# Kernel optimization log

Hardware: AMD Instinct MI355X
Metric: run time of the kernel (lower is better)

Reference implementation:

```python
import jax, jax.numpy as jnp
import numpy as np

N_QUBITS = 9
N_LAYERS = 4
EPS = 1e-5


def _apply_ry(state, wire, theta):
    # state: [N, 2**n] real; theta: [N] or scalar
    n = N_QUBITS
    N = state.shape[0]
    left, right = 2 ** wire, 2 ** (n - 1 - wire)
    s = state.reshape(N, left, 2, right)
    th = jnp.broadcast_to(jnp.asarray(theta, state.dtype), (N,))[:, None, None]
    c, si = jnp.cos(th / 2), jnp.sin(th / 2)
    a, b = s[:, :, 0, :], s[:, :, 1, :]
    out = jnp.stack([c * a - si * b, si * a + c * b], axis=2)
    return out.reshape(N, -1)


def _apply_cnot(state, ctrl, tgt):
    n = N_QUBITS
    N = state.shape[0]
    s = state.reshape((N,) + (2,) * n)
    ca, ta = ctrl + 1, tgt + 1
    sub = jnp.take(s, 1, axis=ca)          # control == 1 slice
    ta2 = ta - 1 if ta > ca else ta
    sub = jnp.flip(sub, axis=ta2)          # X on target
    idx = [slice(None)] * (n + 1)
    idx[ca] = 1
    s = s.at[tuple(idx)].set(sub)
    return s.reshape(N, -1)


def quantum_layer(inputs, q_weights):
    # inputs: [N, n_qubits] angles; q_weights: [n_layers, n_qubits]
    N = inputs.shape[0]
    state = jnp.zeros((N, 2 ** N_QUBITS), inputs.dtype).at[:, 0].set(1.0)
    for i in range(N_QUBITS):
        state = _apply_ry(state, i, inputs[:, i])
    for j in range(N_LAYERS):
        for i in range(N_QUBITS):
            state = _apply_cnot(state, i, (i + 1) % N_QUBITS)
        for i in range(N_QUBITS):
            state = _apply_ry(state, i, q_weights[j, i])
    probs = (state * state).reshape((N,) + (2,) * N_QUBITS)
    zs = []
    for i in range(N_QUBITS):
        axes = tuple(a for a in range(1, N_QUBITS + 1) if a != i + 1)
        p = probs.sum(axes)                # [N, 2]
        zs.append(p[:, 0] - p[:, 1])
    return jnp.stack(zs, axis=1)           # [N, n_qubits]


def _bn(x):
    mu = x.mean((0, 2, 3), keepdims=True)
    var = x.var((0, 2, 3), keepdims=True)
    return (x - mu) * jax.lax.rsqrt(var + EPS)


def _maxpool(x, kh, kw):
    return jax.lax.reduce_window(x, -jnp.inf, jax.lax.max,
                                 (1, 1, kh, kw), (1, 1, kh, kw), 'VALID')


def _conv(x, w):
    return jax.lax.conv_general_dilated(x, w, (1, 1), 'VALID',
                                        dimension_numbers=('NCHW', 'OIHW', 'NCHW'))


def _forward(x, w_conv1, w_conv2, w_conv3, q_weights, fc_w, fc_b):
    h = jax.nn.elu(_bn(_conv(x, w_conv1)))
    h = jnp.pad(h, ((0, 0), (0, 0), (0, 1), (16, 17)))     # ZeroPad2d(16,17,0,1)
    h = _maxpool(jax.nn.elu(_bn(_conv(h, w_conv2))), 2, 4)
    h = jnp.pad(h, ((0, 0), (0, 0), (4, 3), (2, 1)))       # ZeroPad2d(2,1,4,3)
    h = _maxpool(jax.nn.elu(_bn(_conv(h, w_conv3))), 2, 4)
    B, C = h.shape[0], h.shape[1]
    feats = h.reshape(B, C, -1)                            # [B, 32, 9]
    q = quantum_layer(feats.reshape(B * C, N_QUBITS), q_weights)
    q = q.reshape(B, C * N_QUBITS)                         # channel-major concat
    return q @ fc_w.T + fc_b


def setup_inputs() -> dict:
    key = jax.random.key(0)
    ks = jax.random.split(key, 7)
    return {
        'x': jax.random.normal(ks[0], (1024, 1, 4, 216), jnp.float32),
        'w_conv1': jax.random.normal(ks[1], (16, 1, 1, 64), jnp.float32) * 0.05,
        'w_conv2': jax.random.normal(ks[2], (32, 16, 2, 32), jnp.float32) * 0.05,
        'w_conv3': jax.random.normal(ks[3], (32, 32, 8, 4), jnp.float32) * 0.05,
        'q_weights': jax.random.uniform(ks[4], (N_LAYERS, N_QUBITS), jnp.float32, 0.0, 2 * np.pi),
        'fc_w': jax.random.normal(ks[5], (5, 32 * N_QUBITS), jnp.float32) * 0.05,
        'fc_b': jnp.zeros((5,), jnp.float32),
    }


def reference(x, w_conv1, w_conv2, w_conv3, q_weights, fc_w, fc_b):
    return _forward(x, w_conv1, w_conv2, w_conv3, q_weights, fc_w, fc_b)
```

## Files before the change

### kernel.cpp

```cpp
#include <hip/hip_runtime.h>
#include <math.h>

#define NB 1024
#define C1 16
#define H1 4
#define W1 153
#define WX 216
#define K1 64
#define C2 32
#define H2 4
#define W2 155
#define W192 192
#define PW2 38
#define C3 32
#define W3 38

typedef short short4v __attribute__((ext_vector_type(4)));
typedef short short8 __attribute__((ext_vector_type(8)));
typedef float f32x16 __attribute__((ext_vector_type(16)));

#define OFF_OUT1     0
#define OFF_A1H      10027008
#define OFF_A1L      16318464
#define OFF_W2PH     22609920
#define OFF_W2PL     22626304
#define OFF_W3PH     22642688
#define OFF_W3PL     22659072
#define OFF_UH       22675456
#define OFF_UL       22806528
#define OFF_POOL2RAW 22937600
#define OFF_A2H      25427968
#define OFF_A2L      27787264
#define OFF_FEATSRAW 30146560
#define OFF_QO       30441472
#define OFF_PART1    30736384
#define OFF_PART2    30867456
#define OFF_PART3    30998528
#define OFF_STATS1   31031296
#define OFF_STATS2   31031328
#define OFF_STATS3   31031392

__device__ __forceinline__ float eluf(float x){ return x > 0.f ? x : expm1f(x); }

__device__ __forceinline__ ushort bf16h(float x){
  unsigned u = __float_as_uint(x);
  unsigned r = u + 0x7fffu + ((u >> 16) & 1u);
  return (ushort)(r >> 16);
}
__device__ __forceinline__ float bf16f(ushort h){ return __uint_as_float(((unsigned)h) << 16); }

__device__ __forceinline__ short8 cat8(short4v a, short4v b){
  return __builtin_shufflevector(a, b, 0,1,2,3,4,5,6,7);
}

__global__ __launch_bounds__(256) void k_conv1s(const float* __restrict__ x,
                                                const float* __restrict__ w1,
                                                float* __restrict__ out1,
                                                float* __restrict__ part1){
  __shared__ float xr[4][WX];
  __shared__ float wl[C1*K1];
  int n = blockIdx.x, tid = threadIdx.x;
  for (int i = tid; i < 4*WX; i += 256) xr[i/WX][i%WX] = x[(size_t)n*4*WX + i];
  for (int i = tid; i < C1*K1; i += 256) wl[i] = w1[i];
  __syncthreads();
  int h = tid >> 6, lane = tid & 63;
  float acc[16][3];
  #pragma unroll
  for (int c = 0; c < 16; ++c){ acc[c][0]=0.f; acc[c][1]=0.f; acc[c][2]=0.f; }
  bool v2 = (lane + 128) < W1;
  for (int k = 0; k < 64; ++k){
    float x0 = xr[h][lane + k];
    float x1 = xr[h][lane + 64 + k];
    float x2 = v2 ? xr[h][lane + 128 + k] : 0.f;
    #pragma unroll
    for (int c = 0; c < 16; ++c){
      float wk = wl[c*64 + k];
      acc[c][0] += wk*x0; acc[c][1] += wk*x1; acc[c][2] += wk*x2;
    }
  }
  float ss[16], sq[16];
  #pragma unroll
  for (int c = 0; c < 16; ++c){
    float* ob = out1 + (((size_t)(n*16 + c)*4 + h))*W1;
    ob[lane] = acc[c][0];
    ob[lane + 64] = acc[c][1];
    if (v2) ob[lane + 128] = acc[c][2];
    ss[c] = acc[c][0] + acc[c][1] + acc[c][2];
    sq[c] = acc[c][0]*acc[c][0] + acc[c][1]*acc[c][1] + acc[c][2]*acc[c][2];
  }
  #pragma unroll
  for (int m = 1; m < 64; m <<= 1){
    #pragma unroll
    for (int c = 0; c < 16; ++c){ ss[c] += __shfl_xor(ss[c], m); sq[c] += __shfl_xor(sq[c], m); }
  }
  if (lane == 0){
    #pragma unroll
    for (int c = 0; c < 16; ++c){
      part1[((size_t)(n*4 + h)*16 + c)*2]     = ss[c];
      part1[((size_t)(n*4 + h)*16 + c)*2 + 1] = sq[c];
    }
  }
}

__global__ __launch_bounds__(256) void k_stats_finP(const float* __restrict__ part,
                                                    float* __restrict__ stats,
                                                    int C, int nblk, float inv){
  __shared__ float rs[256], rq[256];
  int c = blockIdx.x;
  float s = 0.f, q = 0.f;
  for (int b = threadIdx.x; b < nblk; b += 256){
    s += part[((size_t)b*C + c)*2];
    q += part[((size_t)b*C + c)*2 + 1];
  }
  rs[threadIdx.x] = s; rq[threadIdx.x] = q; __syncthreads();
  for (int st = 128; st > 0; st >>= 1){
    if (threadIdx.x < st){ rs[threadIdx.x] += rs[threadIdx.x+st]; rq[threadIdx.x] += rq[threadIdx.x+st]; }
    __syncthreads();
  }
  if (threadIdx.x == 0){
    float mean = rs[0]*inv;
    float var  = rq[0]*inv - mean*mean;
    stats[c*2]   = mean;
    stats[c*2+1] = rsqrtf(var + 1e-5f);
  }
}

__global__ __launch_bounds__(256) void k_bnelu1(const float* __restrict__ out1,
                                                const float* __restrict__ stats,
                                                ushort* __restrict__ a1h, ushort* __restrict__ a1l){
  __shared__ float xf[2448];
  __shared__ float st[32];
  int b = blockIdx.x;
  int n = b >> 2, h = b & 3;
  int tid = threadIdx.x;
  if (tid < 32) st[tid] = stats[tid];
  for (int i = tid; i < 2448; i += 256){
    int ci = i / 153, w = i - ci*153;
    xf[i] = out1[((size_t)(n*16 + ci)*4 + h)*W1 + w];
  }
  __syncthreads();
  for (int i = tid; i < 3072; i += 256){
    int w = i >> 4, ci = i & 15;
    float v = 0.f;
    int ws = w - 16;
    if ((unsigned)ws < (unsigned)W1){
      float xx = xf[ci*153 + ws];
      v = eluf((xx - st[ci*2])*st[ci*2+1]);
    }
    int ciS = ci ^ (((w >> 2) & 3) << 2);
    size_t o = (size_t)b*3072 + w*16 + ciS;
    ushort hs = bf16h(v);
    a1h[o] = hs;
    a1l[o] = bf16h(v - bf16f(hs));
  }
}

__global__ void k_cvtw(const float* __restrict__ w2, const float* __restrict__ w3,
                       ushort* __restrict__ w2ph, ushort* __restrict__ w2pl,
                       ushort* __restrict__ w3ph, ushort* __restrict__ w3pl){
  int idx = blockIdx.x*256 + threadIdx.x;
  if (idx < 32768){
    int ci = idx & 15; int co = (idx >> 4) & 31; int rk = idx >> 9;
    int r = rk >> 5, kw = rk & 31;
    float v = w2[((size_t)(co*16 + ci)*2 + r)*32 + kw];
    ushort hs = bf16h(v); float hf = bf16f(hs);
    w2ph[idx] = hs; w2pl[idx] = bf16h(v - hf);
  } else {
    int j = idx - 32768;
    int ci = j & 31; int co = (j >> 5) & 31; int rk = j >> 10;
    int r = rk >> 2, kw = rk & 3;
    float v = w3[((size_t)(co*32 + ci)*8 + r)*4 + kw];
    ushort hs = bf16h(v); float hf = bf16f(hs);
    w3ph[j] = hs; w3pl[j] = bf16h(v - hf);
  }
}

template<int HG, int PS>
__device__ __forceinline__ void conv2_body(const ushort* s_hi, const ushort* s_lo,
                                           const ushort* __restrict__ w2ph,
                                           const ushort* __restrict__ w2pl,
                                           float* __restrict__ pool2raw,
                                           float (*statW)[32][2],
                                           int n, int l31, int l5){
  constexpr int P0 = PS ? 3 : 0;
  constexpr int NP = PS ? 2 : 3;
  constexpr int NR = (HG == 0) ? 3 : 2;

  f32x16 acc[2][NP];
  #pragma unroll
  for (int lh = 0; lh < 2; ++lh)
    #pragma unroll
    for (int p = 0; p < NP; ++p)
      #pragma unroll
      for (int e = 0; e < 16; ++e) acc[lh][p][e] = 0.f;

  for (int kw = 0; kw < 32; ++kw){
    short8 Ah[2], Al[2];
    #pragma unroll
    for (int r = 0; r < 2; ++r){
      int widx = ((r*32 + kw)*32 + l31)*16 + l5*4;
      Ah[r] = cat8(*(const short4v*)(w2ph + widx), *(const short4v*)(w2ph + widx + 8));
      Al[r] = cat8(*(const short4v*)(w2pl + widx), *(const short4v*)(w2pl + widx + 8));
    }
    #pragma unroll
    for (int j = 0; j < NR; ++j){
      int rb = (2*HG + j)*3072;
      short8 bh[NP], bl[NP];
      #pragma unroll
      for (int p = 0; p < NP; ++p){
        int pos = (P0 + p)*32 + l31 + kw;
        int sw = ((pos >> 2) & 3) << 2;
        int off0 = rb + pos*16 + ((l5*4) ^ sw);
        int off1 = rb + pos*16 + ((l5*4 + 8) ^ sw);
        bh[p] = cat8(*(const short4v*)(s_hi + off0), *(const short4v*)(s_hi + off1));
        bl[p] = cat8(*(const short4v*)(s_lo + off0), *(const short4v*)(s_lo + off1));
      }
      #pragma unroll
      for (int lh = 0; lh < 2; ++lh){
        #pragma unroll
        for (int r = 0; r < 2; ++r){
          if (lh + r != j) continue;
          #pragma unroll
          for (int p = 0; p < NP; ++p){
            acc[lh][p] = __builtin_amdgcn_mfma_f32_32x32x16_bf16(Ah[r], bh[p], acc[lh][p], 0, 0, 0);
            acc[lh][p] = __builtin_amdgcn_mfma_f32_32x32x16_bf16(Ah[r], bl[p], acc[lh][p], 0, 0, 0);
            acc[lh][p] = __builtin_amdgcn_mfma_f32_32x32x16_bf16(Al[r], bh[p], acc[lh][p], 0, 0, 0);
          }
        }
      }
    }
  }

  {
    float sreg[16], qreg[16];
    #pragma unroll
    for (int e = 0; e < 16; ++e){ sreg[e] = 0.f; qreg[e] = 0.f; }
    #pragma unroll
    for (int lh = 0; lh < 2; ++lh){
      #pragma unroll
      for (int p = 0; p < NP; ++p){
        bool pv = ((P0 + p) < 4) || (l31 < 27);
        #pragma unroll
        for (int e = 0; e < 16; ++e){
          float v = pv ? acc[lh][p][e] : 0.f;
          sreg[e] += v; qreg[e] += v*v;
        }
      }
    }
    #pragma unroll
    for (int m = 1; m < 32; m <<= 1){
      #pragma unroll
      for (int e = 0; e < 16; ++e){
        sreg[e] += __shfl_xor(sreg[e], m);
        qreg[e] += __shfl_xor(qreg[e], m);
      }
    }
    if (l31 == 0){
      #pragma unroll
      for (int e = 0; e < 16; ++e){
        int co = (e & 3) + ((e >> 2) << 3) + (l5 << 2);
        statW[HG*2 + PS][co][0] = sreg[e];
        statW[HG*2 + PS][co][1] = qreg[e];
      }
    }
  }
  #pragma unroll
  for (int p = 0; p < NP; ++p){
    #pragma unroll
    for (int e = 0; e < 16; ++e){
      float m0 = fmaxf(acc[0][p][e], acc[1][p][e]);
      float v1 = fmaxf(m0, __shfl_xor(m0, 1));
      float v2m = fmaxf(v1, __shfl_xor(v1, 2));
      int pw = (P0 + p)*8 + (l31 >> 2);
      if ((l31 & 3) == 0 && pw < PW2){
        int co = (e & 3) + ((e >> 2) << 3) + (l5 << 2);
        pool2raw[(((size_t)n*2 + HG)*32 + co)*PW2 + pw] = v2m;
      }
    }
  }
}

__global__ __launch_bounds__(256) void k_conv2f(const ushort* __restrict__ a1h,
                                                const ushort* __restrict__ a1l,
                                                const ushort* __restrict__ w2ph,
                                                const ushort* __restrict__ w2pl,
                                                float* __restrict__ pool2raw,
                                                float* __restrict__ part2){
  __shared__ __align__(16) ushort s_hi[4*3072];
  __shared__ __align__(16) ushort s_lo[4*3072];
  __shared__ float statW[4][32][2];
  int n = blockIdx.x;
  int tid = threadIdx.x;
  {
    const float4* gh = (const float4*)(a1h + (size_t)n*12288);
    const float4* gl = (const float4*)(a1l + (size_t)n*12288);
    float4* dh = (float4*)s_hi;
    float4* dl = (float4*)s_lo;
    #pragma unroll
    for (int i = 0; i < 6; ++i){ dh[tid + 256*i] = gh[tid + 256*i]; dl[tid + 256*i] = gl[tid + 256*i]; }
  }
  __syncthreads();
  int wv = tid >> 6, lane = tid & 63;
  int l5 = lane >> 5, l31 = lane & 31;
  int role = (wv + n) & 3;
  switch (role){
    case 0: conv2_body<0,0>(s_hi, s_lo, w2ph, w2pl, pool2raw, statW, n, l31, l5); break;
    case 1: conv2_body<0,1>(s_hi, s_lo, w2ph, w2pl, pool2raw, statW, n, l31, l5); break;
    case 2: conv2_body<1,0>(s_hi, s_lo, w2ph, w2pl, pool2raw, statW, n, l31, l5); break;
    default: conv2_body<1,1>(s_hi, s_lo, w2ph, w2pl, pool2raw, statW, n, l31, l5); break;
  }
  __syncthreads();
  if (tid < 64){
    int hg = tid >> 5, co = tid & 31;
    float s = statW[hg*2][co][0] + statW[hg*2 + 1][co][0];
    float q = statW[hg*2][co][1] + statW[hg*2 + 1][co][1];
    part2[(((size_t)n*2 + hg)*32 + co)*2]     = s;
    part2[(((size_t)n*2 + hg)*32 + co)*2 + 1] = q;
  }
}

__global__ __launch_bounds__(256) void k_bn2(const float* __restrict__ pool2raw,
                                             const float* __restrict__ stats,
                                             ushort* __restrict__ a2h, ushort* __restrict__ a2l){
  __shared__ float xf[1216];
  __shared__ float st[64];
  int b = blockIdx.x;
  int tid = threadIdx.x;
  if (tid < 64) st[tid] = stats[tid];
  for (int i = tid; i < 1216; i += 256) xf[i] = pool2raw[(size_t)b*1216 + i];
  __syncthreads();
  for (int i = tid; i < 2304; i += 256){
    int w = i >> 5, ci = i & 31;
    float v = 0.f;
    int pw = w - 2;
    if ((unsigned)pw < (unsigned)PW2)
      v = eluf((xf[ci*38 + pw] - st[ci*2])*st[ci*2+1]);
    int ciS = ci ^ (((w >> 1) & 7) << 2);
    size_t o = (size_t)b*2304 + w*32 + ciS;
    ushort hs = bf16h(v);
    a2h[o] = hs; a2l[o] = bf16h(v - bf16f(hs));
  }
}

__global__ __launch_bounds__(256, 2) void k_conv3f(const ushort* __restrict__ a2h,
                                                   const ushort* __restrict__ a2l,
                                                   const ushort* __restrict__ w3ph,
                                                   const ushort* __restrict__ w3pl,
                                                   float* __restrict__ featsraw,
                                                   float* __restrict__ part3){
  __shared__ __align__(16) ushort s3h[9216];
  __shared__ __align__(16) ushort s3l[9216];
  __shared__ float poolL3[4][32][12];
  __shared__ float statL3[4][32][2];
  int nb = blockIdx.x;
  int tid = threadIdx.x;
  {
    const float4* gh = (const float4*)(a2h + (size_t)nb*9216);
    const float4* gl = (const float4*)(a2l + (size_t)nb*9216);
    float4* dh = (float4*)s3h;
    float4* dl = (float4*)s3l;
    for (int i = tid; i < 1152; i += 256){ dh[i] = gh[i]; dl[i] = gl[i]; }
  }
  __syncthreads();
  int wave = tid >> 6, lane = tid & 63;
  int nh = wave >> 1, h = wave & 1;
  int l5 = lane >> 5, l31 = lane & 31;

  f32x16 acc[2];
  #pragma unroll
  for (int p = 0; p < 2; ++p)
    #pragma unroll
    for (int e = 0; e < 16; ++e) acc[p][e] = 0.f;

  #pragma unroll
  for (int ri = 0; ri < 2; ++ri){
    int r = (h == 0) ? (4 + ri) : (3 + ri);
    int rbase = (nh*2 + ri)*72*32;
    #pragma unroll
    for (int kw = 0; kw < 4; ++kw){
      #pragma unroll
      for (int ch = 0; ch < 2; ++ch){
        int widx = ((r*4 + kw)*32 + l31)*32 + ch*16 + l5*4;
        short8 Ah = cat8(*(const short4v*)(w3ph + widx), *(const short4v*)(w3ph + widx + 8));
        short8 Al = cat8(*(const short4v*)(w3pl + widx), *(const short4v*)(w3pl + widx + 8));
        short8 Bh[2], Bl[2];
        #pragma unroll
        for (int p = 0; p < 2; ++p){
          int pos = p*32 + l31 + kw;
          int sw = ((pos >> 1) & 7) << 2;
          int s0 = ch*16 + l5*4;
          int off0 = rbase + pos*32 + (s0 ^ sw);
          int off1 = rbase + pos*32 + ((s0 + 8) ^ sw);
          Bh[p] = cat8(*(const short4v*)(s3h + off0), *(const short4v*)(s3h + off1));
          Bl[p] = cat8(*(const short4v*)(s3l + off0), *(const short4v*)(s3l + off1));
        }
        #pragma unroll
        for (int p = 0; p < 2; ++p) acc[p] = __builtin_amdgcn_mfma_f32_32x32x16_bf16(Ah, Bh[p], acc[p], 0, 0, 0);
        #pragma unroll
        for (int p = 0; p < 2; ++p) acc[p] = __builtin_amdgcn_mfma_f32_32x32x16_bf16(Ah, Bl[p], acc[p], 0, 0, 0);
        #pragma unroll
        for (int p = 0; p < 2; ++p) acc[p] = __builtin_amdgcn_mfma_f32_32x32x16_bf16(Al, Bh[p], acc[p], 0, 0, 0);
      }
    }
  }

  {
    float sreg[16], qreg[16];
    #pragma unroll
    for (int e = 0; e < 16; ++e){ sreg[e] = 0.f; qreg[e] = 0.f; }
    #pragma unroll
    for (int p = 0; p < 2; ++p){
      bool pv = (p == 0) || (l31 < 6);
      #pragma unroll
      for (int e = 0; e < 16; ++e){
        float v = pv ? acc[p][e] : 0.f;
        sreg[e] += v; qreg[e] += v*v;
      }
    }
    #pragma unroll
    for (int m = 1; m < 32; m <<= 1){
      #pragma unroll
      for (int e = 0; e < 16; ++e){
        sreg[e] += __shfl_xor(sreg[e], m);
        qreg[e] += __shfl_xor(qreg[e], m);
      }
    }
    if (l31 == 0){
      #pragma unroll
      for (int e = 0; e < 16; ++e){
        int co = (e & 3) + ((e >> 2) << 3) + (l5 << 2);
        statL3[wave][co][0] = sreg[e];
        statL3[wave][co][1] = qreg[e];
      }
    }
  }
  #pragma unroll
  for (int p = 0; p < 2; ++p){
    #pragma unroll
    for (int e = 0; e < 16; ++e){
      float v = acc[p][e];
      float v1 = fmaxf(v, __shfl_xor(v, 1));
      float v2m = fmaxf(v1, __shfl_xor(v1, 2));
      int pw = p*8 + (l31 >> 2);
      if ((l31 & 3) == 0 && pw < 9){
        int co = (e & 3) + ((e >> 2) << 3) + (l5 << 2);
        poolL3[wave][co][pw] = v2m;
      }
    }
  }
  __syncthreads();
  for (int i = tid; i < 2*32*9; i += 256){
    int pw = i % 9; int t = i / 9; int co = t & 31; int nh2 = t >> 5;
    float v = fmaxf(poolL3[nh2*2][co][pw], poolL3[nh2*2+1][co][pw]);
    featsraw[((size_t)(nb*2 + nh2)*32 + co)*9 + pw] = v;
  }
  if (tid < 32){
    float s = 0.f, q = 0.f;
    #pragma unroll
    for (int wv = 0; wv < 4; ++wv){ s += statL3[wv][tid][0]; q += statL3[wv][tid][1]; }
    part3[((size_t)nb*32 + tid)*2]     = s;
    part3[((size_t)nb*32 + tid)*2 + 1] = q;
  }
}

__global__ __launch_bounds__(256) void k_buildU(const float* __restrict__ qw,
                                                ushort* __restrict__ Uh, ushort* __restrict__ Ul){
  __shared__ float wt[36][2];
  int tid = threadIdx.x;
  if (tid < 36){ float s, c; sincosf(qw[tid]*0.5f, &s, &c); wt[tid][0] = c; wt[tid][1] = s; }
  __syncthreads();
  int wid = tid >> 6, lane = tid & 63;
  int k = blockIdx.x*4 + wid;
  float v[8];
  #pragma unroll
  for (int r = 0; r < 8; ++r) v[r] = (lane*8 + r == k) ? 1.f : 0.f;

  for (int j = 0; j < 4; ++j){
    #pragma unroll
    for (int i = 0; i < 5; ++i){
      int cm = 32>>i, tm = 16>>i;
      bool flip = (lane & cm) != 0;
      #pragma unroll
      for (int r = 0; r < 8; ++r){
        float w = __shfl_xor(v[r], tm);
        v[r] = flip ? w : v[r];
      }
    }
    { bool flip = (lane & 1) != 0;
      #pragma unroll
      for (int r = 0; r < 4; ++r){ float a = v[r], bb = v[r+4]; v[r] = flip?bb:a; v[r+4] = flip?a:bb; } }
    { float t = v[4]; v[4] = v[6]; v[6] = t; t = v[5]; v[5] = v[7]; v[7] = t; }
    { float t = v[2]; v[2] = v[3]; v[3] = t; t = v[6]; v[6] = v[7]; v[7] = t; }
    #pragma unroll
    for (int r = 1; r < 8; r += 2) v[r] = __shfl_xor(v[r], 32);

    #pragma unroll
    for (int i = 0; i < 6; ++i){
      float c = wt[j*9+i][0], s = wt[j*9+i][1];
      int m = 32>>i;
      float sg = (lane & m) ? s : -s;
      #pragma unroll
      for (int r = 0; r < 8; ++r){
        float w = __shfl_xor(v[r], m);
        v[r] = c*v[r] + sg*w;
      }
    }
    { float c = wt[j*9+6][0], s = wt[j*9+6][1];
      #pragma unroll
      for (int r = 0; r < 4; ++r){ float a = v[r], bb = v[r+4]; v[r] = c*a - s*bb; v[r+4] = s*a + c*bb; } }
    { float c = wt[j*9+7][0], s = wt[j*9+7][1]; float a, bb;
      a=v[0]; bb=v[2]; v[0]=c*a-s*bb; v[2]=s*a+c*bb;
      a=v[1]; bb=v[3]; v[1]=c*a-s*bb; v[3]=s*a+c*bb;
      a=v[4]; bb=v[6]; v[4]=c*a-s*bb; v[6]=s*a+c*bb;
      a=v[5]; bb=v[7]; v[5]=c*a-s*bb; v[7]=s*a+c*bb; }
    { float c = wt[j*9+8][0], s = wt[j*9+8][1]; float a, bb;
      a=v[0]; bb=v[1]; v[0]=c*a-s*bb; v[1]=s*a+c*bb;
      a=v[2]; bb=v[3]; v[2]=c*a-s*bb; v[3]=s*a+c*bb;
      a=v[4]; bb=v[5]; v[4]=c*a-s*bb; v[5]=s*a+c*bb;
      a=v[6]; bb=v[7]; v[6]=c*a-s*bb; v[7]=s*a+c*bb; }
  }
  #pragma unroll
  for (int r = 0; r < 8; ++r){
    int s = lane*8 + r;
    int mf = s >> 5, r31 = s & 31;
    int addr = (((k >> 4)*16 + mf)*32 + r31)*16 + (k & 15);
    float f = v[r];
    ushort hi = bf16h(f);
    Uh[addr] = hi;
    Ul[addr] = bf16h(f - bf16f(hi));
  }
}

__global__ __launch_bounds__(256, 1) void k_qgemm(const float* __restrict__ featsraw,
                                                  const float* __restrict__ stats,
                                                  const ushort* __restrict__ Uh,
                                                  const ushort* __restrict__ Ul,
                                                  float* __restrict__ qo){
  __shared__ __align__(16) ushort BhL[32768];
  __shared__ __align__(16) ushort BlL[32768];
  __shared__ float angL[576];
  __shared__ float zred[4][64][9];
  int nb = blockIdx.x;
  int tid = threadIdx.x;
  for (int t = tid; t < 576; t += 256){
    float vr = featsraw[(size_t)nb*576 + t];
    int c = (t/9) & 31;
    angL[t] = 0.5f * eluf((vr - stats[c*2])*stats[c*2+1]);
  }
  __syncthreads();
  {
    int sm = tid >> 2, q = tid & 3;
    float tc[9], ts[9];
    #pragma unroll
    for (int i = 0; i < 9; ++i) sincosf(angL[sm*9 + i], &ts[i], &tc[i]);
    float Pc = ((q & 2) ? ts[0] : tc[0]) * ((q & 1) ? ts[1] : tc[1]);
    int swz = (sm >> 2) & 3;
    short4v* bh4 = (short4v*)BhL;
    short4v* bl4 = (short4v*)BlL;
    int j = 0;
    #pragma unroll
    for (int b2 = 0; b2 < 2; ++b2){ float p2 = Pc*(b2 ? ts[2] : tc[2]);
    #pragma unroll
    for (int b3 = 0; b3 < 2; ++b3){ float p3 = p2*(b3 ? ts[3] : tc[3]);
    #pragma unroll
    for (int b4 = 0; b4 < 2; ++b4){ float p4 = p3*(b4 ? ts[4] : tc[4]);
    #pragma unroll
    for (int b5 = 0; b5 < 2; ++b5){ float p5 = p4*(b5 ? ts[5] : tc[5]);
    #pragma unroll
    for (int b6 = 0; b6 < 2; ++b6){ float p6 = p5*(b6 ? ts[6] : tc[6]);
      float a0 = p6*tc[7]*tc[8];
      float a1 = p6*tc[7]*ts[8];
      float a2 = p6*ts[7]*tc[8];
      float a3 = p6*ts[7]*ts[8];
      ushort h0 = bf16h(a0), h1 = bf16h(a1), h2 = bf16h(a2), h3 = bf16h(a3);
      short4v hv; hv[0]=(short)h0; hv[1]=(short)h1; hv[2]=(short)h2; hv[3]=(short)h3;
      short4v lv; lv[0]=(short)bf16h(a0 - bf16f(h0)); lv[1]=(short)bf16h(a1 - bf16f(h1));
                  lv[2]=(short)bf16h(a2 - bf16f(h2)); lv[3]=(short)bf16h(a3 - bf16f(h3));
      int kk = q*128 + j;
      int kstep = kk >> 4;
      int g = (kk >> 2) & 3;
      int idx4 = (kstep*64 + sm)*4 + (g ^ swz);
      bh4[idx4] = hv; bl4[idx4] = lv;
      j += 4;
    }}}}}
  }
  __syncthreads();
  int wv = tid >> 6, lane = tid & 63, l5 = lane >> 5, l31 = lane & 31;
  f32x16 acc[4][2];
  #pragma unroll
  for (int jj = 0; jj < 4; ++jj)
    #pragma unroll
    for (int nf = 0; nf < 2; ++nf)
      #pragma unroll
      for (int e = 0; e < 16; ++e) acc[jj][nf][e] = 0.f;

  for (int kstep = 0; kstep < 32; ++kstep){
    short8 Bh[2], Bl[2];
    #pragma unroll
    for (int nf = 0; nf < 2; ++nf){
      int sm = nf*32 + l31;
      int base = (kstep*64 + sm)*16;
      int sz = ((sm >> 2) & 3) << 2;
      int e0 = (l5*4) ^ sz;
      int e1 = (l5*4 + 8) ^ sz;
      Bh[nf] = cat8(*(const short4v*)(BhL + base + e0), *(const short4v*)(BhL + base + e1));
      Bl[nf] = cat8(*(const short4v*)(BlL + base + e0), *(const short4v*)(BlL + base + e1));
    }
    #pragma unroll
    for (int jj = 0; jj < 4; ++jj){
      int mf = wv*4 + jj;
      const ushort* ah = Uh + ((kstep*16 + mf)*32 + l31)*16 + l5*4;
      const ushort* al = Ul + ((kstep*16 + mf)*32 + l31)*16 + l5*4;
      short8 Ah = cat8(*(const short4v*)ah, *(const short4v*)(ah + 8));
      short8 Al = cat8(*(const short4v*)al, *(const short4v*)(al + 8));
      acc[jj][0] = __builtin_amdgcn_mfma_f32_32x32x16_bf16(Ah, Bh[0], acc[jj][0], 0, 0, 0);
      acc[jj][1] = __builtin_amdgcn_mfma_f32_32x32x16_bf16(Ah, Bh[1], acc[jj][1], 0, 0, 0);
      acc[jj][0] = __builtin_amdgcn_mfma_f32_32x32x16_bf16(Ah, Bl[0], acc[jj][0], 0, 0, 0);
      acc[jj][1] = __builtin_amdgcn_mfma_f32_32x32x16_bf16(Ah, Bl[1], acc[jj][1], 0, 0, 0);
      acc[jj][0] = __builtin_amdgcn_mfma_f32_32x32x16_bf16(Al, Bh[0], acc[jj][0], 0, 0, 0);
      acc[jj][1] = __builtin_amdgcn_mfma_f32_32x32x16_bf16(Al, Bh[1], acc[jj][1], 0, 0, 0);
    }
  }
  float zz[2][9];
  #pragma unroll
  for (int nf = 0; nf < 2; ++nf)
    #pragma unroll
    for (int i = 0; i < 9; ++i) zz[nf][i] = 0.f;
  #pragma unroll
  for (int jj = 0; jj < 4; ++jj){
    int mf = wv*4 + jj;
    float sg0 = (mf & 8) ? -1.f : 1.f;
    float sg1 = (mf & 4) ? -1.f : 1.f;
    float sg2 = (mf & 2) ? -1.f : 1.f;
    float sg3 = (mf & 1) ? -1.f : 1.f;
    #pragma unroll
    for (int nf = 0; nf < 2; ++nf){
      float psum = 0.f, z4 = 0.f, z5 = 0.f, z7 = 0.f, z8 = 0.f;
      #pragma unroll
      for (int e = 0; e < 16; ++e){
        float qv = acc[jj][nf][e]*acc[jj][nf][e];
        psum += qv;
        z4 += ((e >> 3) & 1) ? -qv : qv;
        z5 += ((e >> 2) & 1) ? -qv : qv;
        z7 += ((e >> 1) & 1) ? -qv : qv;
        z8 += (e & 1) ? -qv : qv;
      }
      zz[nf][0] += sg0*psum; zz[nf][1] += sg1*psum;
      zz[nf][2] += sg2*psum; zz[nf][3] += sg3*psum;
      zz[nf][4] += z4; zz[nf][5] += z5;
      zz[nf][6] += l5 ? -psum : psum;
      zz[nf][7] += z7; zz[nf][8] += z8;
    }
  }
  #pragma unroll
  for (int nf = 0; nf < 2; ++nf)
    #pragma unroll
    for (int i = 0; i < 9; ++i) zz[nf][i] += __shfl_xor(zz[nf][i], 32);
  if (l5 == 0){
    #pragma unroll
    for (int nf = 0; nf < 2; ++nf)
      #pragma unroll
      for (int i = 0; i < 9; ++i) zred[wv][nf*32 + l31][i] = zz[nf][i];
  }
  __syncthreads();
  for (int t = tid; t < 576; t += 256){
    int sm = t / 9, i = t - sm*9;
    float s = zred[0][sm][i] + zred[1][sm][i] + zred[2][sm][i] + zred[3][sm][i];
    qo[(size_t)(nb*64 + sm)*9 + i] = s;
  }
}

__global__ void k_fc(const float* __restrict__ q, const float* __restrict__ fw,
                     const float* __restrict__ fb, float* __restrict__ out){
  int idx = blockIdx.x*256 + threadIdx.x;
  if (idx >= NB*5) return;
  int b = idx / 5, o = idx - b*5;
  const float* qr = q + (size_t)b*288;
  const float* wr = fw + (size_t)o*288;
  float s = 0.f;
  for (int j = 0; j < 288; ++j) s += qr[j]*wr[j];
  out[idx] = s + fb[o];
}

extern "C" void kernel_launch(void* const* d_in, const int* in_sizes, int n_in,
                              void* d_out, int out_size, void* d_ws, size_t ws_size,
                              hipStream_t stream){
  const float* x  = (const float*)d_in[0];
  const float* w1 = (const float*)d_in[1];
  const float* w2 = (const float*)d_in[2];
  const float* w3 = (const float*)d_in[3];
  const float* qw = (const float*)d_in[4];
  const float* fw = (const float*)d_in[5];
  const float* fb = (const float*)d_in[6];
  float* out = (float*)d_out;
  float* W = (float*)d_ws;

  float*  out1   = W + OFF_OUT1;
  ushort* a1h    = (ushort*)(W + OFF_A1H);
  ushort* a1l    = (ushort*)(W + OFF_A1L);
  ushort* w2ph   = (ushort*)(W + OFF_W2PH);
  ushort* w2pl   = (ushort*)(W + OFF_W2PL);
  ushort* w3ph   = (ushort*)(W + OFF_W3PH);
  ushort* w3pl   = (ushort*)(W + OFF_W3PL);
  ushort* uH     = (ushort*)(W + OFF_UH);
  ushort* uL     = (ushort*)(W + OFF_UL);
  float*  pool2raw = W + OFF_POOL2RAW;
  ushort* a2h    = (ushort*)(W + OFF_A2H);
  ushort* a2l    = (ushort*)(W + OFF_A2L);
  float*  featsraw = W + OFF_FEATSRAW;
  float*  qo     = W + OFF_QO;
  float*  part1  = W + OFF_PART1;
  float*  part2  = W + OFF_PART2;
  float*  part3  = W + OFF_PART3;
  float*  stats1 = W + OFF_STATS1;
  float*  stats2 = W + OFF_STATS2;
  float*  stats3 = W + OFF_STATS3;

  k_conv1s<<<NB, 256, 0, stream>>>(x, w1, out1, part1);
  k_stats_finP<<<16, 256, 0, stream>>>(part1, stats1, 16, NB*4, 1.f/((float)NB*H1*W1));
  k_bnelu1<<<NB*4, 256, 0, stream>>>(out1, stats1, a1h, a1l);
  k_cvtw<<<256, 256, 0, stream>>>(w2, w3, w2ph, w2pl, w3ph, w3pl);
  k_buildU<<<128, 256, 0, stream>>>(qw, uH, uL);
  k_conv2f<<<NB, 256, 0, stream>>>(a1h, a1l, w2ph, w2pl, pool2raw, part2);
  k_stats_finP<<<32, 256, 0, stream>>>(part2, stats2, 32, NB*2, 1.f/((float)NB*H2*W2));
  k_bn2<<<NB*2, 256, 0, stream>>>(pool2raw, stats2, a2h, a2l);
  k_conv3f<<<NB/2, 256, 0, stream>>>(a2h, a2l, w3ph, w3pl, featsraw, part3);
  k_stats_finP<<<32, 256, 0, stream>>>(part3, stats3, 32, NB/2, 1.f/((float)NB*2*W3));
  k_qgemm<<<NB/2, 256, 0, stream>>>(featsraw, stats3, uH, uL, qo);
  k_fc<<<20, 256, 0, stream>>>(qo, fw, fb, out);
}
```

Before: 338.2 us.

## Split conv2 blocks per height group and widen LDS loads to 16 bytes

The conv2 kernel now launches two blocks per sample, one per output height group. Each block loads only the 3 or 2 input rows it needs into LDS, so shared memory per block shrinks and occupancy can rise. The position tiles are spread across four waves per block with finer granularity. The LDS swizzle is changed to an 8-element XOR so the A and B operands load as single 16-byte short8 reads instead of two 8-byte reads. The risk is redundant staging of the overlapping middle row and uneven work among the four waves.

```diff
diff --git a/kernel.cpp b/kernel.cpp
--- a/kernel.cpp
+++ b/kernel.cpp
@@ -147,7 +147,7 @@
       float xx = xf[ci*153 + ws];
       v = eluf((xx - st[ci*2])*st[ci*2+1]);
     }
-    int ciS = ci ^ (((w >> 2) & 3) << 2);
+    int ciS = ci ^ (((w >> 2) & 1) << 3);
     size_t o = (size_t)b*3072 + w*16 + ciS;
     ushort hs = bf16h(v);
     a1h[o] = hs;
@@ -182,9 +182,10 @@
                                            float* __restrict__ pool2raw,
                                            float (*statW)[32][2],
                                            int n, int l31, int l5){
-  constexpr int P0 = PS ? 3 : 0;
-  constexpr int NP = PS ? 2 : 3;
+  constexpr int P0 = (PS == 0) ? 0 : (PS + 1);
+  constexpr int NP = (PS == 0) ? 2 : 1;
   constexpr int NR = (HG == 0) ? 3 : 2;
+  int e8 = l5*8;
 
   f32x16 acc[2][NP];
   #pragma unroll
@@ -198,22 +199,20 @@
     short8 Ah[2], Al[2];
     #pragma unroll
     for (int r = 0; r < 2; ++r){
-      int widx = ((r*32 + kw)*32 + l31)*16 + l5*4;
-      Ah[r] = cat8(*(const short4v*)(w2ph + widx), *(const short4v*)(w2ph + widx + 8));
-      Al[r] = cat8(*(const short4v*)(w2pl + widx), *(const short4v*)(w2pl + widx + 8));
+      int widx = ((r*32 + kw)*32 + l31)*16 + e8;
+      Ah[r] = *(const short8*)(w2ph + widx);
+      Al[r] = *(const short8*)(w2pl + widx);
     }
     #pragma unroll
     for (int j = 0; j < NR; ++j){
-      int rb = (2*HG + j)*3072;
+      int rb = j*3072;
       short8 bh[NP], bl[NP];
       #pragma unroll
       for (int p = 0; p < NP; ++p){
         int pos = (P0 + p)*32 + l31 + kw;
-        int sw = ((pos >> 2) & 3) << 2;
-        int off0 = rb + pos*16 + ((l5*4) ^ sw);
-        int off1 = rb + pos*16 + ((l5*4 + 8) ^ sw);
-        bh[p] = cat8(*(const short4v*)(s_hi + off0), *(const short4v*)(s_hi + off1));
-        bl[p] = cat8(*(const short4v*)(s_lo + off0), *(const short4v*)(s_lo + off1));
+        int off = rb + pos*16 + (e8 ^ (((pos >> 2) & 1) << 3));
+        bh[p] = *(const short8*)(s_hi + off);
+        bl[p] = *(const short8*)(s_lo + off);
       }
       #pragma unroll
       for (int lh = 0; lh < 2; ++lh){
@@ -259,8 +258,8 @@
       #pragma unroll
       for (int e = 0; e < 16; ++e){
         int co = (e & 3) + ((e >> 2) << 3) + (l5 << 2);
-        statW[HG*2 + PS][co][0] = sreg[e];
-        statW[HG*2 + PS][co][1] = qreg[e];
+        statW[PS][co][0] = sreg[e];
+        statW[PS][co][1] = qreg[e];
       }
     }
   }
@@ -280,42 +279,52 @@
   }
 }
 
-__global__ __launch_bounds__(256) void k_conv2f(const ushort* __restrict__ a1h,
-                                                const ushort* __restrict__ a1l,
-                                                const ushort* __restrict__ w2ph,
-                                                const ushort* __restrict__ w2pl,
-                                                float* __restrict__ pool2raw,
-                                                float* __restrict__ part2){
-  __shared__ __align__(16) ushort s_hi[4*3072];
-  __shared__ __align__(16) ushort s_lo[4*3072];
+__global__ __launch_bounds__(256, 4) void k_conv2f(const ushort* __restrict__ a1h,
+                                                   const ushort* __restrict__ a1l,
+                                                   const ushort* __restrict__ w2ph,
+                                                   const ushort* __restrict__ w2pl,
+                                                   float* __restrict__ pool2raw,
+                                                   float* __restrict__ part2){
+  __shared__ __align__(16) ushort s_hi[3*3072];
+  __shared__ __align__(16) ushort s_lo[3*3072];
   __shared__ float statW[4][32][2];
-  int n = blockIdx.x;
+  int b = blockIdx.x;
+  int n = b >> 1, HG = b & 1;
   int tid = threadIdx.x;
+  int nrows = HG ? 2 : 3;
   {
-    const float4* gh = (const float4*)(a1h + (size_t)n*12288);
-    const float4* gl = (const float4*)(a1l + (size_t)n*12288);
+    const float4* gh = (const float4*)(a1h + ((size_t)n*4 + 2*HG)*3072);
+    const float4* gl = (const float4*)(a1l + ((size_t)n*4 + 2*HG)*3072);
     float4* dh = (float4*)s_hi;
     float4* dl = (float4*)s_lo;
-    #pragma unroll
-    for (int i = 0; i < 6; ++i){ dh[tid + 256*i] = gh[tid + 256*i]; dl[tid + 256*i] = gl[tid + 256*i]; }
+    int cnt = nrows*384;
+    for (int i = tid; i < cnt; i += 256){ dh[i] = gh[i]; dl[i] = gl[i]; }
   }
   __syncthreads();
   int wv = tid >> 6, lane = tid & 63;
   int l5 = lane >> 5, l31 = lane & 31;
-  int role = (wv + n) & 3;
-  switch (role){
-    case 0: conv2_body<0,0>(s_hi, s_lo, w2ph, w2pl, pool2raw, statW, n, l31, l5); break;
-    case 1: conv2_body<0,1>(s_hi, s_lo, w2ph, w2pl, pool2raw, statW, n, l31, l5); break;
-    case 2: conv2_body<1,0>(s_hi, s_lo, w2ph, w2pl, pool2raw, statW, n, l31, l5); break;
-    default: conv2_body<1,1>(s_hi, s_lo, w2ph, w2pl, pool2raw, statW, n, l31, l5); break;
-  }
-  __syncthreads();
-  if (tid < 64){
-    int hg = tid >> 5, co = tid & 31;
-    float s = statW[hg*2][co][0] + statW[hg*2 + 1][co][0];
-    float q = statW[hg*2][co][1] + statW[hg*2 + 1][co][1];
-    part2[(((size_t)n*2 + hg)*32 + co)*2]     = s;
-    part2[(((size_t)n*2 + hg)*32 + co)*2 + 1] = q;
+  int ps = (wv + b) & 3;
+  if (HG == 0){
+    switch (ps){
+      case 0: conv2_body<0,0>(s_hi, s_lo, w2ph, w2pl, pool2raw, statW, n, l31, l5); break;
+      case 1: conv2_body<0,1>(s_hi, s_lo, w2ph, w2pl, pool2raw, statW, n, l31, l5); break;
+      case 2: conv2_body<0,2>(s_hi, s_lo, w2ph, w2pl, pool2raw, statW, n, l31, l5); break;
+      default: conv2_body<0,3>(s_hi, s_lo, w2ph, w2pl, pool2raw, statW, n, l31, l5); break;
+    }
+  } else {
+    switch (ps){
+      case 0: conv2_body<1,0>(s_hi, s_lo, w2ph, w2pl, pool2raw, statW, n, l31, l5); break;
+      case 1: conv2_body<1,1>(s_hi, s_lo, w2ph, w2pl, pool2raw, statW, n, l31, l5); break;
+      case 2: conv2_body<1,2>(s_hi, s_lo, w2ph, w2pl, pool2raw, statW, n, l31, l5); break;
+      default: conv2_body<1,3>(s_hi, s_lo, w2ph, w2pl, pool2raw, statW, n, l31, l5); break;
+    }
+  }
+  __syncthreads();
+  if (tid < 32){
+    float s = statW[0][tid][0] + statW[1][tid][0] + statW[2][tid][0] + statW[3][tid][0];
+    float q = statW[0][tid][1] + statW[1][tid][1] + statW[2][tid][1] + statW[3][tid][1];
+    part2[(((size_t)n*2 + HG)*32 + tid)*2]     = s;
+    part2[(((size_t)n*2 + HG)*32 + tid)*2 + 1] = q;
   }
 }
 
@@ -721,7 +730,7 @@
   k_bnelu1<<<NB*4, 256, 0, stream>>>(out1, stats1, a1h, a1l);
   k_cvtw<<<256, 256, 0, stream>>>(w2, w3, w2ph, w2pl, w3ph, w3pl);
   k_buildU<<<128, 256, 0, stream>>>(qw, uH, uL);
-  k_conv2f<<<NB, 256, 0, stream>>>(a1h, a1l, w2ph, w2pl, pool2raw, part2);
+  k_conv2f<<<NB*2, 256, 0, stream>>>(a1h, a1l, w2ph, w2pl, pool2raw, part2);
   k_stats_finP<<<32, 256, 0, stream>>>(part2, stats2, 32, NB*2, 1.f/((float)NB*H2*W2));
   k_bn2<<<NB*2, 256, 0, stream>>>(pool2raw, stats2, a2h, a2l);
   k_conv3f<<<NB/2, 256, 0, stream>>>(a2h, a2l, w3ph, w3pl, featsraw, part3);
```

Result: faster. 316.3 us (median of 2 runs) (-6.5%).
